# Kernel optimization log

Hardware: AMD Instinct MI355X
Metric: run time of the kernel (lower is better)

Reference implementation:

```python
import jax, jax.numpy as jnp
from jax import lax
import numpy as np

B, T, D_IN = 4, 1024, 8
D_MODEL, N_LAYERS, HORIZON, D_OUT = 512, 2, 24, 8
D_STATE, D_CONV, EXPAND = 64, 4, 2
D_INNER = EXPAND * D_MODEL
DT_RANK = -(-D_MODEL // 16)  # ceil(d_model/16) = 32
LN_EPS = 1e-5


def setup_inputs() -> dict:
    key = jax.random.key(0)
    ks = iter(jax.random.split(key, 24))
    rn = lambda shape, s: jax.random.normal(next(ks), shape, jnp.float32) * s
    A_log = jnp.tile(jnp.log(jnp.arange(1, D_STATE + 1, dtype=jnp.float32)), (N_LAYERS, D_INNER, 1))
    return {
        "x": rn((B, T, D_IN), 1.0),
        "W_in": rn((D_IN, D_MODEL), 0.3), "b_in": jnp.zeros((D_MODEL,), jnp.float32),
        "W_xz": rn((N_LAYERS, D_MODEL, 2 * D_INNER), 0.04),
        "conv_w": rn((N_LAYERS, D_INNER, D_CONV), 0.3), "conv_b": jnp.zeros((N_LAYERS, D_INNER), jnp.float32),
        "W_xproj": rn((N_LAYERS, D_INNER, DT_RANK + 2 * D_STATE), 0.03),
        "W_dt": rn((N_LAYERS, DT_RANK, D_INNER), 0.1), "b_dt": rn((N_LAYERS, D_INNER), 0.1) - 4.0,
        "A_log": A_log, "D_skip": jnp.ones((N_LAYERS, D_INNER), jnp.float32),
        "W_out": rn((N_LAYERS, D_INNER, D_MODEL), 0.03),
        "ln_g": jnp.ones((D_MODEL,), jnp.float32), "ln_b": jnp.zeros((D_MODEL,), jnp.float32),
        "W_h1": rn((D_MODEL, D_MODEL), 0.04), "b_h1": jnp.zeros((D_MODEL,), jnp.float32),
        "W_h2": rn((D_MODEL, HORIZON * D_OUT), 0.04), "b_h2": jnp.zeros((HORIZON * D_OUT,), jnp.float32),
    }


def mamba_block(h, Wxz, cw, cb, Wxp, Wdt, bdt, Alog, Dsk, Wout):
    # h: [B,T,d_model] -> [B,T,d_model]  (mamba-ssm Mamba block, no residual)
    xz = h @ Wxz                                   # [B,T,2*d_inner]
    xb, z = jnp.split(xz, 2, axis=-1)
    # depthwise causal conv over time
    xc = jnp.transpose(xb, (0, 2, 1))              # [B,d_inner,T]
    xc = lax.conv_general_dilated(xc, cw[:, None, :], (1,), [(D_CONV - 1, 0)],
                                  feature_group_count=D_INNER)
    xc = jax.nn.silu(xc + cb[None, :, None])
    xc = jnp.transpose(xc, (0, 2, 1))              # [B,T,d_inner]
    # input-dependent dt, B, C
    xdb = xc @ Wxp                                 # [B,T,dt_rank+2*d_state]
    dt_r = xdb[..., :DT_RANK]
    Bc = xdb[..., DT_RANK:DT_RANK + D_STATE]
    Cc = xdb[..., DT_RANK + D_STATE:]
    dt = jax.nn.softplus(dt_r @ Wdt + bdt)         # [B,T,d_inner]
    A = -jnp.exp(Alog)                             # [d_inner,d_state]

    def step(hst, ins):
        dt_t, B_t, C_t, x_t = ins                  # [B,d_inner],[B,N],[B,N],[B,d_inner]
        dA = jnp.exp(dt_t[..., None] * A)          # [B,d_inner,N]
        hst = dA * hst + dt_t[..., None] * B_t[:, None, :] * x_t[..., None]
        y = jnp.einsum('bdn,bn->bd', hst, C_t)
        return hst, y

    h0 = jnp.zeros((h.shape[0], D_INNER, D_STATE), h.dtype)
    xs = (jnp.transpose(dt, (1, 0, 2)), jnp.transpose(Bc, (1, 0, 2)),
          jnp.transpose(Cc, (1, 0, 2)), jnp.transpose(xc, (1, 0, 2)))
    _, ys = lax.scan(step, h0, xs)                 # ys: [T,B,d_inner]
    y = jnp.transpose(ys, (1, 0, 2)) + Dsk * xc
    y = y * jax.nn.silu(z)
    return y @ Wout


def reference(x, W_in, b_in, W_xz, conv_w, conv_b, W_xproj, W_dt, b_dt, A_log, D_skip,
              W_out, ln_g, ln_b, W_h1, b_h1, W_h2, b_h2):
    h = x @ W_in + b_in                            # [B,T,d_model]
    for i in range(N_LAYERS):
        h = mamba_block(h, W_xz[i], conv_w[i], conv_b[i], W_xproj[i], W_dt[i],
                        b_dt[i], A_log[i], D_skip[i], W_out[i])
    mu = jnp.mean(h, axis=-1, keepdims=True)
    var = jnp.mean(jnp.square(h - mu), axis=-1, keepdims=True)
    h = (h - mu) * lax.rsqrt(var + LN_EPS) * ln_g + ln_b
    last = h[:, -1, :]                             # [B,d_model]
    hid = jax.nn.gelu(last @ W_h1 + b_h1, approximate=False)
    yhat = hid @ W_h2 + b_h2                       # [B,horizon*d_out]
    return yhat.reshape(x.shape[0], HORIZON, D_OUT)
```

## Files before the change

kernel.cpp:

```cpp
#include <hip/hip_runtime.h>
#include <hip/hip_bf16.h>

static constexpr int kB      = 4;
static constexpr int kT      = 1024;
static constexpr int kDIN    = 8;
static constexpr int kDMODEL = 512;
static constexpr int kHOR    = 24;
static constexpr int kDOUT   = 8;
static constexpr int kDSTATE = 64;
static constexpr int kDINNER = 1024;
static constexpr int kDTRANK = 32;
static constexpr int kXPROJ  = 160;
static constexpr int kXPAD   = 256;
static constexpr int kBT     = kB * kT;
static constexpr int kNLAYER = 2;

typedef __bf16 bf16x8 __attribute__((ext_vector_type(8)));
typedef float  f32x4  __attribute__((ext_vector_type(4)));

__device__ __forceinline__ float silu_f(float x)     { return x / (1.f + __expf(-x)); }
__device__ __forceinline__ float softplus_f(float x) { return (x > 20.f) ? x : log1pf(__expf(x)); }
__device__ __forceinline__ float gelu_f(float x)     { return 0.5f * x * (1.f + erff(x * 0.70710678118654752f)); }

__device__ __forceinline__ void gld_lds16(const void* g, void* l) {
    __builtin_amdgcn_global_load_lds(
        (const __attribute__((address_space(1))) unsigned int*)g,
        (__attribute__((address_space(3))) unsigned int*)l, 16, 0, 0);
}

template<int CTRL>
__device__ __forceinline__ float dpp_mov(float v) {
    return __int_as_float(__builtin_amdgcn_update_dpp(
        0, __float_as_int(v), CTRL, 0xf, 0xf, false));
}

__global__ __launch_bounds__(256) void wtrans_all_kernel(
    const float* __restrict__ Wxz, const float* __restrict__ Wxp,
    const float* __restrict__ Wdt, const float* __restrict__ Wout,
    __hip_bfloat16* __restrict__ oxz, __hip_bfloat16* __restrict__ oxp,
    __hip_bfloat16* __restrict__ odt, __hip_bfloat16* __restrict__ oout)
{
    __shared__ float tile[32][33];
    const int bid = blockIdx.x;
    const int tid = threadIdx.x;

    const float* in; __hip_bfloat16* out;
    int K, N, Kpad, TX, loc;
    if (bid < 2048) {
        int l = bid >> 10; loc = bid & 1023;
        in = Wxz + (size_t)l * 512 * 2048; out = oxz + (size_t)l * 2048 * 512;
        K = 512; N = 2048; Kpad = 512; TX = 64;
    } else if (bid < 2368) {
        int r = bid - 2048; int l = r / 160; loc = r % 160;
        in = Wxp + (size_t)l * 1024 * 160; out = oxp + (size_t)l * 256 * 1024;
        K = 1024; N = 160; Kpad = 1024; TX = 5;
    } else if (bid < 2496) {
        int r = bid - 2368; int l = r >> 6; loc = r & 63;
        in = Wdt + (size_t)l * 32 * 1024; out = odt + (size_t)l * 1024 * 64;
        K = 32; N = 1024; Kpad = 64; TX = 32;
    } else {
        int r = bid - 2496; int l = r >> 9; loc = r & 511;
        in = Wout + (size_t)l * 1024 * 512; out = oout + (size_t)l * 512 * 1024;
        K = 1024; N = 512; Kpad = 1024; TX = 16;
    }
    const int n0 = (loc % TX) * 32;
    const int k0 = (loc / TX) * 32;

#pragma unroll
    for (int p = 0; p < 4; ++p) {
        int idx = p * 256 + tid;
        int ki = idx >> 5, ni = idx & 31;
        float v = 0.f;
        if (k0 + ki < K && n0 + ni < N) v = in[(size_t)(k0 + ki) * N + n0 + ni];
        tile[ki][ni] = v;
    }
    __syncthreads();
#pragma unroll
    for (int p = 0; p < 4; ++p) {
        int idx = p * 256 + tid;
        int ni = idx >> 5, ki = idx & 31;
        if (n0 + ni < N)
            out[(size_t)(n0 + ni) * Kpad + k0 + ki] = __float2bfloat16(tile[ki][ni]);
    }
}

template<int MODE, int BN>
__global__ __launch_bounds__(256) void mfma_gemm_bt(
    const __hip_bfloat16* __restrict__ A, int lda,
    const __hip_bfloat16* __restrict__ BT, int ldb,
    const float* __restrict__ bias,
    float* __restrict__ C, int ldc,
    void* __restrict__ C2,
    int K)
{
    __shared__ __align__(16) __hip_bfloat16 sA[128][64];
    __shared__ __align__(16) __hip_bfloat16 sB[BN][64];

    const int tid  = threadIdx.x;
    const int lane = tid & 63;
    const int w    = tid >> 6;
    const int m0   = blockIdx.y * 128;
    const int n0   = blockIdx.x * BN;

    constexpr int NJ = 4;
    constexpr int MI = (BN == 128) ? 4 : 2;
    const int wm = (BN == 128) ? (w >> 1) : w;
    const int wn = (BN == 128) ? (w & 1) : 0;
    const int wmrows = (BN == 128) ? 64 : 32;

    f32x4 acc[MI][NJ] = {};

    const int lrow = lane & 15;
    const int lk   = (lane >> 4) << 3;

    const int grow = tid >> 3;
    const int gcol = (tid & 7) * 8;
    char* ldsA = (char*)&sA[0][0] + w * 1024;
    char* ldsB = (char*)&sB[0][0] + w * 1024;

    for (int k0 = 0; k0 < K; k0 += 64) {
        __syncthreads();
#pragma unroll
        for (int p = 0; p < 4; ++p)
            gld_lds16(A + (size_t)(m0 + grow + p * 32) * lda + k0 + gcol, ldsA + p * 4096);
#pragma unroll
        for (int p = 0; p < BN / 32; ++p)
            gld_lds16(BT + (size_t)(n0 + grow + p * 32) * ldb + k0 + gcol, ldsB + p * 4096);
        __syncthreads();
#pragma unroll
        for (int ks = 0; ks < 2; ++ks) {
            bf16x8 af[MI], bfr[NJ];
#pragma unroll
            for (int i = 0; i < MI; ++i)
                af[i] = *reinterpret_cast<const bf16x8*>(&sA[wm * wmrows + i * 16 + lrow][ks * 32 + lk]);
#pragma unroll
            for (int j = 0; j < NJ; ++j)
                bfr[j] = *reinterpret_cast<const bf16x8*>(&sB[wn * 64 + j * 16 + lrow][ks * 32 + lk]);
#pragma unroll
            for (int i = 0; i < MI; ++i)
#pragma unroll
                for (int j = 0; j < NJ; ++j)
                    acc[i][j] = __builtin_amdgcn_mfma_f32_16x16x32_bf16(af[i], bfr[j], acc[i][j], 0, 0, 0);
        }
    }

    const int crow = (lane >> 4) * 4;
    const int ccol = lane & 15;
#pragma unroll
    for (int i = 0; i < MI; ++i) {
#pragma unroll
        for (int j = 0; j < NJ; ++j) {
#pragma unroll
            for (int r = 0; r < 4; ++r) {
                int row = m0 + wm * wmrows + i * 16 + crow + r;
                int col = n0 + wn * 64 + j * 16 + ccol;
                float v = acc[i][j][r];
                if (MODE == 1) {
                    C[(size_t)row * ldc + col] = v;
                    ((__hip_bfloat16*)C2)[(size_t)row * ldc + col] = __float2bfloat16(v);
                } else if (MODE == 2) {
                    C[(size_t)row * ldc + col] = softplus_f(v + bias[col]);
                } else if (MODE == 4) {
                    if (col < kDINNER)
                        ((__hip_bfloat16*)C)[(size_t)row * ldc + col] = __float2bfloat16(v);
                    else
                        ((__hip_bfloat16*)C2)[(size_t)row * ldc + (col - kDINNER)] =
                            __float2bfloat16(silu_f(v));
                } else {
                    if (col < kDTRANK)
                        ((__hip_bfloat16*)C2)[(size_t)row * kXPAD + col] = __float2bfloat16(v);
                    else if (col < kDTRANK + kDSTATE)
                        C[(size_t)(row >> 1) * 256 + (col - kDTRANK) * 4 + (row & 1) * 2] = v;
                    else if (col < kXPROJ)
                        C[(size_t)(row >> 1) * 256 + (col - kDTRANK - kDSTATE) * 4 + (row & 1) * 2 + 1] = v;
                }
            }
        }
    }
}

__global__ __launch_bounds__(256) void in_proj_kernel(
    const float* __restrict__ x, const float* __restrict__ W,
    const float* __restrict__ b,
    float* __restrict__ h, __hip_bfloat16* __restrict__ hb)
{
    int idx = blockIdx.x * 256 + threadIdx.x;
    int n4 = (idx & 127) * 4;
    int m  = idx >> 7;
    float4 acc = *reinterpret_cast<const float4*>(b + n4);
    const float* xr = x + m * kDIN;
#pragma unroll
    for (int k = 0; k < kDIN; ++k) {
        float4 wv = *reinterpret_cast<const float4*>(W + k * kDMODEL + n4);
        float xv = xr[k];
        acc.x = fmaf(xv, wv.x, acc.x);
        acc.y = fmaf(xv, wv.y, acc.y);
        acc.z = fmaf(xv, wv.z, acc.z);
        acc.w = fmaf(xv, wv.w, acc.w);
    }
    *reinterpret_cast<float4*>(h + (size_t)m * kDMODEL + n4) = acc;
    __bf16 o4[4] = {(__bf16)acc.x, (__bf16)acc.y, (__bf16)acc.z, (__bf16)acc.w};
    *reinterpret_cast<ushort4*>(hb + (size_t)m * kDMODEL + n4) =
        *reinterpret_cast<ushort4*>(o4);
}

__global__ __launch_bounds__(256) void conv_silu_kernel(
    const __hip_bfloat16* __restrict__ xb,
    const float* __restrict__ cw, const float* __restrict__ cb,
    __hip_bfloat16* __restrict__ xc)
{
    int idx = blockIdx.x * 256 + threadIdx.x;
    int dg  = (idx & 127) * 8;
    int bt  = idx >> 7;
    int t   = bt & (kT - 1);

    float4 wv[8];
#pragma unroll
    for (int k = 0; k < 8; ++k)
        wv[k] = *reinterpret_cast<const float4*>(cw + (dg + k) * 4);

    float acc[8];
#pragma unroll
    for (int k = 0; k < 8; ++k) acc[k] = cb[dg + k];

    const __hip_bfloat16* base = xb + (size_t)bt * kDINNER + dg;
    {
        bf16x8 v = *reinterpret_cast<const bf16x8*>(base);
#pragma unroll
        for (int k = 0; k < 8; ++k) acc[k] = fmaf((float)v[k], wv[k].w, acc[k]);
    }
    if (t >= 1) {
        bf16x8 v = *reinterpret_cast<const bf16x8*>(base - kDINNER);
#pragma unroll
        for (int k = 0; k < 8; ++k) acc[k] = fmaf((float)v[k], wv[k].z, acc[k]);
    }
    if (t >= 2) {
        bf16x8 v = *reinterpret_cast<const bf16x8*>(base - 2 * kDINNER);
#pragma unroll
        for (int k = 0; k < 8; ++k) acc[k] = fmaf((float)v[k], wv[k].y, acc[k]);
    }
    if (t >= 3) {
        bf16x8 v = *reinterpret_cast<const bf16x8*>(base - 3 * kDINNER);
#pragma unroll
        for (int k = 0; k < 8; ++k) acc[k] = fmaf((float)v[k], wv[k].x, acc[k]);
    }
    bf16x8 o;
#pragma unroll
    for (int k = 0; k < 8; ++k) o[k] = (__bf16)silu_f(acc[k]);
    *reinterpret_cast<bf16x8*>(xc + (size_t)bt * kDINNER + dg) = o;
}

__global__ __launch_bounds__(256, 4) void scan_kernel(
    const float* __restrict__ dt,
    const float* __restrict__ xdbi,
    const __hip_bfloat16* __restrict__ xc,
    const __hip_bfloat16* __restrict__ zs,
    const float* __restrict__ Alog,
    const float* __restrict__ Dsk,
    __hip_bfloat16* __restrict__ yg)
{
    __shared__ __align__(16) float sBC[2][16][64][4];
    __shared__ __align__(16) float sDT[2][16][4][4];

    const int tid  = threadIdx.x;
    const int lane = tid & 63;
    const int w    = tid >> 6;
    const int bb = blockIdx.x;
    const int b  = (bb & 7) >> 1;
    const int d0 = ((bb >> 3) + (bb & 1) * 128) * 4;
    const int d  = d0 + w;

    const float a2  = -__expf(Alog[d * kDSTATE + lane]) * 1.44269504f;
    const float dsk = Dsk[d];
    const size_t rowbase  = (size_t)b * kT;
    const size_t pairbase = (size_t)b * (kT / 2);
    float s = 0.f;

    auto stageBC = [&](int c, int buf) {
        const float* src = xdbi + (pairbase + c * 16 + 4 * w) * 256 + lane * 4;
#pragma unroll
        for (int p = 0; p < 4; ++p)
            gld_lds16(src + p * 256, &sBC[buf][4 * w + p][0][0]);
    };
    const int lp = tid >> 3, lw = (tid >> 1) & 3, lst = tid & 1;
    auto loadDT = [&](int c, float& odt, float& odx) {
        if (tid < 128) {
            size_t g = (rowbase + c * 32 + lp * 2 + lst) * kDINNER + d0 + lw;
            odt = dt[g];
            odx = odt * (float)((const __bf16*)xc)[g];
        }
    };
    auto writeDT = [&](int buf, float vdt, float vdx) {
        if (tid < 128) {
            sDT[buf][lp][lw][lst * 2]     = vdt;
            sDT[buf][lp][lw][lst * 2 + 1] = vdx;
        }
    };
    auto loadEP = [&](int c, float& oxv, float& ozv) {
        size_t g = (rowbase + c * 32 + (lane & 31)) * kDINNER + d;
        oxv = (float)((const __bf16*)xc)[g];
        ozv = (float)((const __bf16*)zs)[g];
    };

    float pdt = 0.f, pdx = 0.f, exv = 0.f, ezv = 0.f;
    stageBC(0, 0);
    loadDT(0, pdt, pdx);
    loadEP(0, exv, ezv);
    writeDT(0, pdt, pdx);
    __syncthreads();

    for (int c = 0; c < kT / 32; ++c) {
        const int buf = c & 1;
        float ndt = 0.f, ndx = 0.f, nxv = 0.f, nzv = 0.f;
        const bool more = (c + 1 < kT / 32);
        if (more) {
            stageBC(c + 1, buf ^ 1);
            loadDT(c + 1, ndt, ndx);
            loadEP(c + 1, nxv, nzv);
        }

        __builtin_amdgcn_s_setprio(1);
        float yv[32];
#pragma unroll
        for (int p = 0; p < 16; ++p) {
            float4 bc = *reinterpret_cast<const float4*>(&sBC[buf][p][lane][0]);
            float4 dd = *reinterpret_cast<const float4*>(&sDT[buf][p][w][0]);
            float dA0 = exp2f(dd.x * a2);
            s = fmaf(dA0, s, dd.y * bc.x);
            yv[2 * p] = s * bc.y;
            float dA1 = exp2f(dd.z * a2);
            s = fmaf(dA1, s, dd.w * bc.z);
            yv[2 * p + 1] = s * bc.w;
        }

#pragma unroll
        for (int m = 0; m < 16; ++m) {
            float av = yv[2 * m], bv = yv[2 * m + 1];
            float cv = (lane & 1) ? bv : av;
            float dv = (lane & 1) ? av : bv;
            yv[m] = cv + dpp_mov<0xB1>(dv);
        }
#pragma unroll
        for (int m = 0; m < 8; ++m) {
            float av = yv[2 * m], bv = yv[2 * m + 1];
            float cv = (lane & 2) ? bv : av;
            float dv = (lane & 2) ? av : bv;
            yv[m] = cv + dpp_mov<0x4E>(dv);
        }
#pragma unroll
        for (int j = 2; j < 5; ++j) {
            const int S = 1 << j;
#pragma unroll
            for (int m = 0; m < (32 >> (j + 1)); ++m) {
                float av = yv[2 * m], bv = yv[2 * m + 1];
                float cv = (lane & S) ? bv : av;
                float dv = (lane & S) ? av : bv;
                yv[m] = cv + __shfl_xor(dv, S, 64);
            }
        }
        float y = yv[0];
        y += __shfl_xor(y, 32, 64);
        __builtin_amdgcn_s_setprio(0);

        float yo = fmaf(dsk, exv, y) * ezv;
        if (lane < 32) {
            size_t g = (rowbase + c * 32 + lane) * kDINNER + d;
            yg[g] = __float2bfloat16(yo);
        }
        if (more) writeDT(buf ^ 1, ndt, ndx);
        __syncthreads();
        exv = nxv; ezv = nzv;
    }
}

__global__ __launch_bounds__(256) void ln_head_kernel(
    const float* __restrict__ h,
    const float* __restrict__ g, const float* __restrict__ be,
    const float* __restrict__ W1, const float* __restrict__ b1,
    const float* __restrict__ W2, const float* __restrict__ b2,
    float* __restrict__ out)
{
    __shared__ float sln[512];
    __shared__ float shid[512];
    __shared__ float sbuf[8];
    const int b = blockIdx.x, tid = threadIdx.x;
    const float* row = h + (size_t)(b * kT + (kT - 1)) * kDMODEL;

    float v0 = row[tid], v1 = row[tid + 256];
    float s = v0 + v1;
    float q = v0 * v0 + v1 * v1;
#pragma unroll
    for (int m = 32; m >= 1; m >>= 1) {
        s += __shfl_xor(s, m, 64);
        q += __shfl_xor(q, m, 64);
    }
    int wid = tid >> 6;
    if ((tid & 63) == 0) { sbuf[wid] = s; sbuf[4 + wid] = q; }
    __syncthreads();
    if (tid == 0) {
        float S = 0.f, Q = 0.f;
        for (int i = 0; i < 4; ++i) { S += sbuf[i]; Q += sbuf[4 + i]; }
        sbuf[0] = S; sbuf[4] = Q;
    }
    __syncthreads();
    float mean = sbuf[0] * (1.f / kDMODEL);
    float var  = sbuf[4] * (1.f / kDMODEL) - mean * mean;
    float inv  = rsqrtf(var + 1e-5f);
    sln[tid]       = (v0 - mean) * inv * g[tid]       + be[tid];
    sln[tid + 256] = (v1 - mean) * inv * g[tid + 256] + be[tid + 256];
    __syncthreads();

    float a0 = b1[tid], a1 = b1[tid + 256];
#pragma unroll 8
    for (int k = 0; k < kDMODEL; ++k) {
        float lv = sln[k];
        a0 = fmaf(lv, W1[(size_t)k * kDMODEL + tid],       a0);
        a1 = fmaf(lv, W1[(size_t)k * kDMODEL + tid + 256], a1);
    }
    shid[tid]       = gelu_f(a0);
    shid[tid + 256] = gelu_f(a1);
    __syncthreads();

    if (tid < kHOR * kDOUT) {
        float acc = b2[tid];
#pragma unroll 8
        for (int k = 0; k < kDMODEL; ++k)
            acc = fmaf(shid[k], W2[(size_t)k * (kHOR * kDOUT) + tid], acc);
        out[b * (kHOR * kDOUT) + tid] = acc;
    }
}

extern "C" void kernel_launch(void* const* d_in, const int* in_sizes, int n_in,
                              void* d_out, int out_size, void* d_ws, size_t ws_size,
                              hipStream_t stream)
{
    const float* x      = (const float*)d_in[0];
    const float* W_in   = (const float*)d_in[1];
    const float* b_in   = (const float*)d_in[2];
    const float* W_xz   = (const float*)d_in[3];
    const float* conv_w = (const float*)d_in[4];
    const float* conv_b = (const float*)d_in[5];
    const float* W_xp   = (const float*)d_in[6];
    const float* W_dt   = (const float*)d_in[7];
    const float* b_dt   = (const float*)d_in[8];
    const float* A_log  = (const float*)d_in[9];
    const float* D_skip = (const float*)d_in[10];
    const float* W_out  = (const float*)d_in[11];
    const float* ln_g   = (const float*)d_in[12];
    const float* ln_b   = (const float*)d_in[13];
    const float* W_h1   = (const float*)d_in[14];
    const float* b_h1   = (const float*)d_in[15];
    const float* W_h2   = (const float*)d_in[16];
    const float* b_h2   = (const float*)d_in[17];
    float* out = (float*)d_out;

    char* p = (char*)d_ws;
    auto alloc = [&](size_t bytes) { char* q = p; p += (bytes + 255) & ~(size_t)255; return q; };
    float*          h       = (float*)         alloc((size_t)kBT * kDMODEL * 4);
    __hip_bfloat16* h_bf    = (__hip_bfloat16*)alloc((size_t)kBT * kDMODEL * 2);
    __hip_bfloat16* xb_bf   = (__hip_bfloat16*)alloc((size_t)kBT * kDINNER * 2);
    __hip_bfloat16* z_bf    = (__hip_bfloat16*)alloc((size_t)kBT * kDINNER * 2);
    __hip_bfloat16* xc_bf   = (__hip_bfloat16*)alloc((size_t)kBT * kDINNER * 2);
    float*          xdbi    = (float*)         alloc((size_t)(kBT / 2) * 256 * 4);
    __hip_bfloat16* xdb_bf  = (__hip_bfloat16*)alloc((size_t)kBT * kXPAD * 2);
    float*          dtb     = (float*)         alloc((size_t)kBT * kDINNER * 4);
    __hip_bfloat16* ys_bf   = (__hip_bfloat16*)alloc((size_t)kBT * kDINNER * 2);
    __hip_bfloat16* wxz_bt  = (__hip_bfloat16*)alloc((size_t)2 * 2048 * 512 * 2);
    __hip_bfloat16* wxp_bt  = (__hip_bfloat16*)alloc((size_t)2 * 256 * 1024 * 2);
    __hip_bfloat16* wdt_bt  = (__hip_bfloat16*)alloc((size_t)2 * 1024 * 64 * 2);
    __hip_bfloat16* wout_bt = (__hip_bfloat16*)alloc((size_t)2 * 512 * 1024 * 2);

    wtrans_all_kernel<<<3520, 256, 0, stream>>>(
        W_xz, W_xp, W_dt, W_out, wxz_bt, wxp_bt, wdt_bt, wout_bt);

    in_proj_kernel<<<(kBT * 128) / 256, 256, 0, stream>>>(x, W_in, b_in, h, h_bf);

    for (int l = 0; l < kNLAYER; ++l) {
        const float* cw_l  = conv_w + (size_t)l * kDINNER * 4;
        const float* cb_l  = conv_b + (size_t)l * kDINNER;
        const float* bdt_l = b_dt   + (size_t)l * kDINNER;
        const float* Al_l  = A_log  + (size_t)l * kDINNER * kDSTATE;
        const float* Dsk_l = D_skip + (size_t)l * kDINNER;
        const __hip_bfloat16* wxz_l  = wxz_bt  + (size_t)l * 2048 * 512;
        const __hip_bfloat16* wxp_l  = wxp_bt  + (size_t)l * 256 * 1024;
        const __hip_bfloat16* wdt_l  = wdt_bt  + (size_t)l * 1024 * 64;
        const __hip_bfloat16* wout_l = wout_bt + (size_t)l * 512 * 1024;

        mfma_gemm_bt<4, 128><<<dim3(16, 32), 256, 0, stream>>>(
            h_bf, kDMODEL, wxz_l, 512, nullptr, (float*)xb_bf, kDINNER, z_bf, kDMODEL);
        conv_silu_kernel<<<(kBT * 128) / 256, 256, 0, stream>>>(xb_bf, cw_l, cb_l, xc_bf);
        mfma_gemm_bt<5, 64><<<dim3(3, 32), 256, 0, stream>>>(
            xc_bf, kDINNER, wxp_l, 1024, nullptr, xdbi, 0, xdb_bf, kDINNER);
        mfma_gemm_bt<2, 128><<<dim3(8, 32), 256, 0, stream>>>(
            xdb_bf, kXPAD, wdt_l, 64, bdt_l, dtb, kDINNER, nullptr, 64);
        scan_kernel<<<kB * kDINNER / 4, 256, 0, stream>>>(
            dtb, xdbi, xc_bf, z_bf, Al_l, Dsk_l, ys_bf);
        mfma_gemm_bt<1, 64><<<dim3(8, 32), 256, 0, stream>>>(
            ys_bf, kDINNER, wout_l, 1024, nullptr, h, kDMODEL, h_bf, kDINNER);
    }

    ln_head_kernel<<<kB, 256, 0, stream>>>(h, ln_g, ln_b, W_h1, b_h1, W_h2, b_h2, out);
}
```

Measured before the change: 487.1 us.

## Fold input projection into first layer's xz GEMM and shrink GEMM tiles

Layer 0's in_proj and xz GEMM are merged algebraically. The folded weight W_in@W_xz0 (plus a bias row) is precomputed once, so xb/z for layer 0 come from a cheap K=8 elementwise kernel instead of a K=512 MFMA GEMM, and the h/h_bf intermediate write is skipped. The GEMM template gains a BM parameter, and several launches now use smaller 128x64 or 64x64 tiles to raise block counts on the many-CU device. Folding in fp32 changes rounding compared with the bf16 path, and the smaller tiles trade some data reuse for parallelism.

```diff
diff --git a/kernel.cpp b/kernel.cpp
--- a/kernel.cpp
+++ b/kernel.cpp
@@ -84,7 +84,77 @@
     }
 }
 
-template<int MODE, int BN>
+__global__ __launch_bounds__(256) void wfold_kernel(
+    const float* __restrict__ Win, const float* __restrict__ bin,
+    const float* __restrict__ Wxz0, float* __restrict__ wf)
+{
+    __shared__ float sred[3][64][9];
+    const int t    = threadIdx.x & 63;
+    const int part = threadIdx.x >> 6;
+    const int col  = blockIdx.x * 64 + t;
+
+    float acc[9];
+#pragma unroll
+    for (int r = 0; r < 9; ++r) acc[r] = 0.f;
+
+    const int k0 = part * 128;
+#pragma unroll 4
+    for (int k = k0; k < k0 + 128; ++k) {
+        float wv = Wxz0[(size_t)k * 2048 + col];
+#pragma unroll
+        for (int r = 0; r < 8; ++r)
+            acc[r] = fmaf(Win[r * kDMODEL + k], wv, acc[r]);
+        acc[8] = fmaf(bin[k], wv, acc[8]);
+    }
+    if (part > 0) {
+#pragma unroll
+        for (int r = 0; r < 9; ++r) sred[part - 1][t][r] = acc[r];
+    }
+    __syncthreads();
+    if (part == 0) {
+#pragma unroll
+        for (int r = 0; r < 9; ++r)
+            wf[(size_t)col * 12 + r] =
+                acc[r] + sred[0][t][r] + sred[1][t][r] + sred[2][t][r];
+    }
+}
+
+__global__ __launch_bounds__(256) void xz0_kernel(
+    const float* __restrict__ x, const float* __restrict__ wf,
+    __hip_bfloat16* __restrict__ xb, __hip_bfloat16* __restrict__ z)
+{
+    int idx = blockIdx.x * 256 + threadIdx.x;
+    int m  = idx >> 9;
+    int n4 = (idx & 511) * 4;
+    const float* xr = x + m * kDIN;
+    float xv[8];
+#pragma unroll
+    for (int r = 0; r < 8; ++r) xv[r] = xr[r];
+
+    float acc[4];
+#pragma unroll
+    for (int c = 0; c < 4; ++c) {
+        const float* w = wf + (size_t)(n4 + c) * 12;
+        float a = w[8];
+#pragma unroll
+        for (int r = 0; r < 8; ++r) a = fmaf(xv[r], w[r], a);
+        acc[c] = a;
+    }
+    __bf16 o4[4];
+    if (n4 < kDINNER) {
+#pragma unroll
+        for (int c = 0; c < 4; ++c) o4[c] = (__bf16)acc[c];
+        *reinterpret_cast<ushort4*>(xb + (size_t)m * kDINNER + n4) =
+            *reinterpret_cast<ushort4*>(o4);
+    } else {
+#pragma unroll
+        for (int c = 0; c < 4; ++c) o4[c] = (__bf16)silu_f(acc[c]);
+        *reinterpret_cast<ushort4*>(z + (size_t)m * kDINNER + n4 - kDINNER) =
+            *reinterpret_cast<ushort4*>(o4);
+    }
+}
+
+template<int MODE, int BM, int BN>
 __global__ __launch_bounds__(256) void mfma_gemm_bt(
     const __hip_bfloat16* __restrict__ A, int lda,
     const __hip_bfloat16* __restrict__ BT, int ldb,
@@ -93,20 +163,23 @@
     void* __restrict__ C2,
     int K)
 {
-    __shared__ __align__(16) __hip_bfloat16 sA[128][64];
+    constexpr int WN  = (BM == 128 && BN == 64) ? 1 : 2;
+    constexpr int WM  = 4 / WN;
+    constexpr int WTM = BM / WM;
+    constexpr int WTN = BN / WN;
+    constexpr int MI  = WTM / 16;
+    constexpr int NJ  = WTN / 16;
+
+    __shared__ __align__(16) __hip_bfloat16 sA[BM][64];
     __shared__ __align__(16) __hip_bfloat16 sB[BN][64];
 
     const int tid  = threadIdx.x;
     const int lane = tid & 63;
     const int w    = tid >> 6;
-    const int m0   = blockIdx.y * 128;
+    const int m0   = blockIdx.y * BM;
     const int n0   = blockIdx.x * BN;
-
-    constexpr int NJ = 4;
-    constexpr int MI = (BN == 128) ? 4 : 2;
-    const int wm = (BN == 128) ? (w >> 1) : w;
-    const int wn = (BN == 128) ? (w & 1) : 0;
-    const int wmrows = (BN == 128) ? 64 : 32;
+    const int wm   = (WN == 1) ? w : (w >> 1);
+    const int wn   = (WN == 1) ? 0 : (w & 1);
 
     f32x4 acc[MI][NJ] = {};
 
@@ -121,7 +194,7 @@
     for (int k0 = 0; k0 < K; k0 += 64) {
         __syncthreads();
 #pragma unroll
-        for (int p = 0; p < 4; ++p)
+        for (int p = 0; p < BM / 32; ++p)
             gld_lds16(A + (size_t)(m0 + grow + p * 32) * lda + k0 + gcol, ldsA + p * 4096);
 #pragma unroll
         for (int p = 0; p < BN / 32; ++p)
@@ -132,10 +205,10 @@
             bf16x8 af[MI], bfr[NJ];
 #pragma unroll
             for (int i = 0; i < MI; ++i)
-                af[i] = *reinterpret_cast<const bf16x8*>(&sA[wm * wmrows + i * 16 + lrow][ks * 32 + lk]);
+                af[i] = *reinterpret_cast<const bf16x8*>(&sA[wm * WTM + i * 16 + lrow][ks * 32 + lk]);
 #pragma unroll
             for (int j = 0; j < NJ; ++j)
-                bfr[j] = *reinterpret_cast<const bf16x8*>(&sB[wn * 64 + j * 16 + lrow][ks * 32 + lk]);
+                bfr[j] = *reinterpret_cast<const bf16x8*>(&sB[wn * WTN + j * 16 + lrow][ks * 32 + lk]);
 #pragma unroll
             for (int i = 0; i < MI; ++i)
 #pragma unroll
@@ -152,8 +225,8 @@
         for (int j = 0; j < NJ; ++j) {
 #pragma unroll
             for (int r = 0; r < 4; ++r) {
-                int row = m0 + wm * wmrows + i * 16 + crow + r;
-                int col = n0 + wn * 64 + j * 16 + ccol;
+                int row = m0 + wm * WTM + i * 16 + crow + r;
+                int col = n0 + wn * WTN + j * 16 + ccol;
                 float v = acc[i][j][r];
                 if (MODE == 1) {
                     C[(size_t)row * ldc + col] = v;
@@ -179,31 +252,6 @@
     }
 }
 
-__global__ __launch_bounds__(256) void in_proj_kernel(
-    const float* __restrict__ x, const float* __restrict__ W,
-    const float* __restrict__ b,
-    float* __restrict__ h, __hip_bfloat16* __restrict__ hb)
-{
-    int idx = blockIdx.x * 256 + threadIdx.x;
-    int n4 = (idx & 127) * 4;
-    int m  = idx >> 7;
-    float4 acc = *reinterpret_cast<const float4*>(b + n4);
-    const float* xr = x + m * kDIN;
-#pragma unroll
-    for (int k = 0; k < kDIN; ++k) {
-        float4 wv = *reinterpret_cast<const float4*>(W + k * kDMODEL + n4);
-        float xv = xr[k];
-        acc.x = fmaf(xv, wv.x, acc.x);
-        acc.y = fmaf(xv, wv.y, acc.y);
-        acc.z = fmaf(xv, wv.z, acc.z);
-        acc.w = fmaf(xv, wv.w, acc.w);
-    }
-    *reinterpret_cast<float4*>(h + (size_t)m * kDMODEL + n4) = acc;
-    __bf16 o4[4] = {(__bf16)acc.x, (__bf16)acc.y, (__bf16)acc.z, (__bf16)acc.w};
-    *reinterpret_cast<ushort4*>(hb + (size_t)m * kDMODEL + n4) =
-        *reinterpret_cast<ushort4*>(o4);
-}
-
 __global__ __launch_bounds__(256) void conv_silu_kernel(
     const __hip_bfloat16* __restrict__ xb,
     const float* __restrict__ cw, const float* __restrict__ cb,
@@ -469,11 +517,11 @@
     __hip_bfloat16* wxp_bt  = (__hip_bfloat16*)alloc((size_t)2 * 256 * 1024 * 2);
     __hip_bfloat16* wdt_bt  = (__hip_bfloat16*)alloc((size_t)2 * 1024 * 64 * 2);
     __hip_bfloat16* wout_bt = (__hip_bfloat16*)alloc((size_t)2 * 512 * 1024 * 2);
+    float*          wfold   = (float*)         alloc((size_t)2048 * 12 * 4);
 
     wtrans_all_kernel<<<3520, 256, 0, stream>>>(
         W_xz, W_xp, W_dt, W_out, wxz_bt, wxp_bt, wdt_bt, wout_bt);
-
-    in_proj_kernel<<<(kBT * 128) / 256, 256, 0, stream>>>(x, W_in, b_in, h, h_bf);
+    wfold_kernel<<<32, 256, 0, stream>>>(W_in, b_in, W_xz, wfold);
 
     for (int l = 0; l < kNLAYER; ++l) {
         const float* cw_l  = conv_w + (size_t)l * kDINNER * 4;
@@ -486,16 +534,20 @@
         const __hip_bfloat16* wdt_l  = wdt_bt  + (size_t)l * 1024 * 64;
         const __hip_bfloat16* wout_l = wout_bt + (size_t)l * 512 * 1024;
 
-        mfma_gemm_bt<4, 128><<<dim3(16, 32), 256, 0, stream>>>(
-            h_bf, kDMODEL, wxz_l, 512, nullptr, (float*)xb_bf, kDINNER, z_bf, kDMODEL);
+        if (l == 0) {
+            xz0_kernel<<<(kBT * 512) / 256, 256, 0, stream>>>(x, wfold, xb_bf, z_bf);
+        } else {
+            mfma_gemm_bt<4, 128, 64><<<dim3(32, 32), 256, 0, stream>>>(
+                h_bf, kDMODEL, wxz_l, 512, nullptr, (float*)xb_bf, kDINNER, z_bf, kDMODEL);
+        }
         conv_silu_kernel<<<(kBT * 128) / 256, 256, 0, stream>>>(xb_bf, cw_l, cb_l, xc_bf);
-        mfma_gemm_bt<5, 64><<<dim3(3, 32), 256, 0, stream>>>(
+        mfma_gemm_bt<5, 64, 64><<<dim3(3, 64), 256, 0, stream>>>(
             xc_bf, kDINNER, wxp_l, 1024, nullptr, xdbi, 0, xdb_bf, kDINNER);
-        mfma_gemm_bt<2, 128><<<dim3(8, 32), 256, 0, stream>>>(
+        mfma_gemm_bt<2, 64, 64><<<dim3(16, 64), 256, 0, stream>>>(
             xdb_bf, kXPAD, wdt_l, 64, bdt_l, dtb, kDINNER, nullptr, 64);
         scan_kernel<<<kB * kDINNER / 4, 256, 0, stream>>>(
             dtb, xdbi, xc_bf, z_bf, Al_l, Dsk_l, ys_bf);
-        mfma_gemm_bt<1, 64><<<dim3(8, 32), 256, 0, stream>>>(
+        mfma_gemm_bt<1, 64, 64><<<dim3(8, 64), 256, 0, stream>>>(
             ys_bf, kDINNER, wout_l, 1024, nullptr, h, kDMODEL, h_bf, kDINNER);
     }
 
```

Measured after the change: 477.2 us. -2.0%, faster.
